# Kernel optimization log

Hardware: AMD Instinct MI355X
Metric: run time of the kernel (lower is better)

The kernel has to match this reference:

```python
import jax, jax.numpy as jnp
import numpy as np

D_MODEL = 2048
N_HEADS = 16
D_HEAD = 128
B = 2
S = 2048


def setup_inputs() -> dict:
    key = jax.random.key(0)
    ks = jax.random.split(key, 9)
    sc_in = 1.0 / np.sqrt(D_MODEL)
    sc_hd = 1.0 / np.sqrt(N_HEADS * D_HEAD)
    return {
        "x": jax.random.normal(ks[0], (B, S, D_MODEL), dtype=jnp.float32),
        "Wq": jax.random.normal(ks[1], (D_MODEL, N_HEADS * D_HEAD), dtype=jnp.float32) * sc_in,
        "bq": jax.random.normal(ks[2], (N_HEADS * D_HEAD,), dtype=jnp.float32) * 0.01,
        "Wk": jax.random.normal(ks[3], (D_MODEL, N_HEADS * D_HEAD), dtype=jnp.float32) * sc_in,
        "bk": jax.random.normal(ks[4], (N_HEADS * D_HEAD,), dtype=jnp.float32) * 0.01,
        "Wv": jax.random.normal(ks[5], (D_MODEL, N_HEADS * D_HEAD), dtype=jnp.float32) * sc_in,
        "bv": jax.random.normal(ks[6], (N_HEADS * D_HEAD,), dtype=jnp.float32) * 0.01,
        "Wo": jax.random.normal(ks[7], (N_HEADS * D_HEAD, D_MODEL), dtype=jnp.float32) * sc_hd,
        "bo": jax.random.normal(ks[8], (D_MODEL,), dtype=jnp.float32) * 0.01,
    }


def reference(x, Wq, bq, Wk, bk, Wv, bv, Wo, bo):
    b, s, _ = x.shape
    # projections -> [b, s, h, d] -> [b, h, s, d]
    q = (x @ Wq + bq).reshape(b, s, N_HEADS, D_HEAD).transpose(0, 2, 1, 3)
    k = (x @ Wk + bk).reshape(b, s, N_HEADS, D_HEAD).transpose(0, 2, 1, 3)
    v = (x @ Wv + bv).reshape(b, s, N_HEADS, D_HEAD).transpose(0, 2, 1, 3)
    scale = 1.0 / jnp.sqrt(jnp.asarray(D_HEAD, dtype=x.dtype))
    scores = jnp.einsum("bhsd,bhtd->bhst", q, k) * scale  # [b,h,s,s]
    causal = jnp.triu(jnp.ones((s, s), dtype=bool), k=1)
    scores = jnp.where(causal, jnp.asarray(-jnp.inf, dtype=scores.dtype), scores)
    attn = jax.nn.softmax(scores, axis=-1)
    ctx = jnp.einsum("bhst,bhtd->bhsd", attn, v)  # [b,h,s,d]
    ctx = ctx.transpose(0, 2, 1, 3).reshape(b, s, N_HEADS * D_HEAD)
    return ctx @ Wo + bo
```

## Files before the change

### kernel.cpp

```cpp
#include <hip/hip_runtime.h>
#include <hip/hip_bf16.h>
#include <stdint.h>

#define S_LEN  2048
#define DMODEL 2048
#define NHEADS 16
#define DHEAD  128
#define NBATCH 2
#define MROWS  (NBATCH * S_LEN)

typedef __bf16 bf16_t;
typedef __bf16 bf16x8 __attribute__((ext_vector_type(8)));
typedef float  f32x4  __attribute__((ext_vector_type(4)));
typedef float  f32x16 __attribute__((ext_vector_type(16)));

#define MFMA_BF16(A, B, C) __builtin_amdgcn_mfma_f32_16x16x32_bf16((A), (B), (C), 0, 0, 0)
#define MFMA32(A, B, C)    __builtin_amdgcn_mfma_f32_32x32x16_bf16((A), (B), (C), 0, 0, 0)

__device__ __forceinline__ void gload_lds16(const void* g, void* l) {
  __builtin_amdgcn_global_load_lds(
      (__attribute__((address_space(1))) uint32_t*)(uintptr_t)g,
      (__attribute__((address_space(3))) uint32_t*)l,
      16, 0, 0);
}

__device__ __forceinline__ unsigned pk2(float lo, float hi) {
  const unsigned short a = __builtin_bit_cast(unsigned short, (bf16_t)lo);
  const unsigned short b = __builtin_bit_cast(unsigned short, (bf16_t)hi);
  return (unsigned)a | ((unsigned)b << 16);
}

__global__ __launch_bounds__(256) void cast_kernel(const float* __restrict__ X,
                                                   bf16_t* __restrict__ Xb) {
  const int i = blockIdx.x * 256 + threadIdx.x;
  const f32x4 a = ((const f32x4*)X)[2 * i];
  const f32x4 b = ((const f32x4*)X)[2 * i + 1];
  bf16x8 o;
#pragma unroll
  for (int j = 0; j < 4; ++j) { o[j] = (bf16_t)a[j]; o[j + 4] = (bf16_t)b[j]; }
  ((bf16x8*)Xb)[i] = o;
}

__global__ __launch_bounds__(256) void transpose_cast(
    const float* __restrict__ W0, const float* __restrict__ W1,
    const float* __restrict__ W2, const float* __restrict__ W3,
    bf16_t* __restrict__ T0, bf16_t* __restrict__ T1,
    bf16_t* __restrict__ T2, bf16_t* __restrict__ T3) {
  const float* W; bf16_t* T;
  switch (blockIdx.z) {
    case 0:  W = W0; T = T0; break;
    case 1:  W = W1; T = T1; break;
    case 2:  W = W2; T = T2; break;
    default: W = W3; T = T3; break;
  }
  __shared__ float tile[64][65];
  const int r0 = blockIdx.y * 64;
  const int c0 = blockIdx.x * 64;
  const int tx = threadIdx.x & 63;
  const int ty = threadIdx.x >> 6;
#pragma unroll
  for (int i = 0; i < 16; ++i) {
    const int r = ty + i * 4;
    tile[r][tx] = W[(size_t)(r0 + r) * DMODEL + c0 + tx];
  }
  __syncthreads();
#pragma unroll
  for (int i = 0; i < 16; ++i) {
    const int r = ty + i * 4;
    T[(size_t)(c0 + r) * DMODEL + r0 + tx] = (bf16_t)tile[tx][r];
  }
}

__global__ __launch_bounds__(256) void transpose_v(const bf16_t* __restrict__ V,
                                                   bf16_t* __restrict__ VT) {
  __shared__ bf16_t tile[64 * 64];
  const int bh = blockIdx.z;
  const int s0 = blockIdx.x * 64;
  const int d0 = blockIdx.y * 64;
  const bf16_t* src = V + ((size_t)bh * S_LEN + s0) * DHEAD + d0;
#pragma unroll
  for (int i = 0; i < 2; ++i) {
    const int v = threadIdx.x + i * 256;
    const int r = v >> 3, ch = v & 7;
    *(bf16x8*)&tile[r * 64 + ((ch ^ ((r >> 3) & 7)) << 3)] =
        *(const bf16x8*)(src + (size_t)r * DHEAD + ch * 8);
  }
  __syncthreads();
  bf16_t* dst = VT + ((size_t)bh * DHEAD + d0) * S_LEN + s0;
#pragma unroll
  for (int i = 0; i < 2; ++i) {
    const int v = threadIdx.x + i * 256;
    const int d = v >> 3, j = v & 7;
    bf16x8 o;
#pragma unroll
    for (int e = 0; e < 8; ++e) {
      const int row = j * 8 + e;
      o[e] = tile[row * 64 + (((d >> 3) ^ j) << 3) + (d & 7)];
    }
    *(bf16x8*)(dst + (size_t)d * S_LEN + j * 8) = o;
  }
}

#define VMCNT(N) asm volatile("s_waitcnt vmcnt(" #N ")" ::: "memory")

#define QPHASE(T, P, N) do {                                                     \
  VMCNT(N);                                                                      \
  __builtin_amdgcn_s_barrier();                                                  \
  asm volatile("" ::: "memory");                                                 \
  {                                                                              \
    const char* regA = lds + ((T) & 1) * 65536 + ((P) >> 1) * 32768;             \
    const char* regB = regA + 16384;                                             \
    if (((P) & 1) == 0) {                                                        \
      _Pragma("unroll")                                                          \
      for (int j = 0; j < 4; ++j)                                                \
        bf[j] = *(const bf16x8*)(regB + (wn * 64 + j * 16 + l16) * 64 + g * 16); \
    }                                                                            \
    bf16x8 af[4];                                                                \
    _Pragma("unroll")                                                            \
    for (int i = 0; i < 4; ++i)                                                  \
      af[i] = *(const bf16x8*)(regA + (wm * 128 + (((P) & 1) * 4 + i) * 16 + l16) * 64 + g * 16); \
    stage((T) + 1, (P));                                                         \
    __builtin_amdgcn_s_setprio(1);                                               \
    _Pragma("unroll")                                                            \
    for (int i = 0; i < 4; ++i) {                                                \
      _Pragma("unroll")                                                          \
      for (int j = 0; j < 4; ++j)                                                \
        acc[((P) & 1) * 4 + i][j] =                                              \
            MFMA_BF16(af[i], bf[j], acc[((P) & 1) * 4 + i][j]);                  \
    }                                                                            \
    __builtin_amdgcn_s_setprio(0);                                               \
  }                                                                              \
} while (0)

__global__ __launch_bounds__(512, 2) void gemm_qkv(
    const bf16_t* __restrict__ Xb,
    const bf16_t* __restrict__ WqT, const bf16_t* __restrict__ WkT,
    const bf16_t* __restrict__ WvT,
    const float* __restrict__ bq, const float* __restrict__ bk,
    const float* __restrict__ bv,
    bf16_t* __restrict__ Qg, bf16_t* __restrict__ Kg, bf16_t* __restrict__ Vg) {
  __shared__ __align__(16) char lds[2 * 65536];

  const int tid  = threadIdx.x;
  const int lane = tid & 63;
  const int w    = tid >> 6;
  const int g    = lane >> 4;
  const int l16  = lane & 15;
  const int wm   = w >> 2;
  const int wn   = w & 3;

  const int bid = blockIdx.x;
  const int wg  = (bid & 7) * 48 + (bid >> 3);
  const int mi  = wg / 24;
  const int ni  = wg % 24;
  const int z0  = ni >> 3;
  const bf16_t* Bt = (z0 == 0) ? WqT : (z0 == 1) ? WkT : WvT;
  const bf16_t* Abase = Xb + (size_t)mi * 256 * DMODEL;
  const bf16_t* Bbase = Bt + (size_t)(ni & 7) * 256 * DMODEL;

  f32x4 acc[8][4];
#pragma unroll
  for (int i = 0; i < 8; ++i)
#pragma unroll
    for (int j = 0; j < 4; ++j) acc[i][j] = (f32x4){0.f, 0.f, 0.f, 0.f};

  auto stage = [&](int tile, int p) {
    if (tile >= DMODEL / 64) return;
    const int kh = p >> 1, mat = p & 1;
    const int kt = tile * 64 + kh * 32;
    const bf16_t* src = mat ? Bbase : Abase;
    char* dstbase = lds + (tile & 1) * 65536 + kh * 32768 + mat * 16384;
#pragma unroll
    for (int jj = 0; jj < 2; ++jj) {
      const int c = jj * 512 + tid;
      gload_lds16(src + (size_t)(c >> 2) * DMODEL + kt + (c & 3) * 8,
                  dstbase + (jj * 512 + (tid & ~63)) * 16);
    }
  };

  stage(0, 0); stage(0, 1); stage(0, 2); stage(0, 3);

  bf16x8 bf[4];
  for (int t = 0; t < DMODEL / 64 - 1; ++t) {
    QPHASE(t, 0, 4);
    QPHASE(t, 1, 6);
    QPHASE(t, 2, 4);
    QPHASE(t, 3, 6);
  }
  {
    const int t = DMODEL / 64 - 1;
    QPHASE(t, 0, 4);
    QPHASE(t, 1, 4);
    QPHASE(t, 2, 2);
    QPHASE(t, 3, 0);
  }

  const float* bias = (z0 == 0) ? bq : (z0 == 1) ? bk : bv;
  bf16_t* outb      = (z0 == 0) ? Qg : (z0 == 1) ? Kg : Vg;
#pragma unroll
  for (int i = 0; i < 8; ++i) {
#pragma unroll
    for (int j = 0; j < 4; ++j) {
      const int nloc = (ni & 7) * 256 + wn * 64 + j * 16 + l16;
      const float bb = bias[nloc];
      const int h = nloc >> 7, d = nloc & (DHEAD - 1);
#pragma unroll
      for (int r = 0; r < 4; ++r) {
        const int mrow = mi * 256 + wm * 128 + i * 16 + g * 4 + r;
        const int b = mrow >> 11, s = mrow & (S_LEN - 1);
        outb[((size_t)(b * NHEADS + h) * S_LEN + s) * DHEAD + d] =
            (bf16_t)(acc[i][j][r] + bb);
      }
    }
  }
}

template <int MODE>
__device__ __forceinline__ void gemm8_body(const bf16_t* __restrict__ A,
                                           const bf16_t* __restrict__ Bt,
                                           const float* __restrict__ bias,
                                           void* __restrict__ out) {
  __shared__ __align__(16) char lds8[2 * 49152];
  const int tid  = threadIdx.x;
  const int lane = tid & 63;
  const int w    = tid >> 6;
  const int g    = lane >> 4;
  const int l16  = lane & 15;
  const int wm   = w >> 2;
  const int wn   = w & 3;
  const int m0   = blockIdx.y * 128;
  const int n0   = blockIdx.x * 256;

  f32x4 acc[4][4];
#pragma unroll
  for (int i = 0; i < 4; ++i)
#pragma unroll
    for (int j = 0; j < 4; ++j) acc[i][j] = (f32x4){0.f, 0.f, 0.f, 0.f};

  const int st_r0 = tid >> 3;
  const int st_ch = tid & 7;

  auto stage = [&](int tile, int r) {
    if (tile >= DMODEL / 64) return;
    const int kt = tile << 6;
    char* db = lds8 + (tile & 1) * 49152 + r * 16384 + w * 1024;
    const bf16_t* sb = (r == 0) ? (A + (size_t)m0 * DMODEL + kt)
                                : (Bt + (size_t)(n0 + ((r - 1) << 7)) * DMODEL + kt);
#pragma unroll
    for (int jj = 0; jj < 2; ++jj) {
      const int row = jj * 64 + st_r0;
      gload_lds16(sb + (size_t)row * DMODEL + ((st_ch ^ (row & 7)) << 3),
                  db + jj * 8192);
    }
  };

  stage(0, 0); stage(0, 1); stage(0, 2); stage(1, 0);
  asm volatile("s_waitcnt vmcnt(2)" ::: "memory");
  __builtin_amdgcn_s_barrier();

#pragma unroll 2
  for (int t = 0; t < DMODEL / 64; ++t) {
    const char* cb = lds8 + (t & 1) * 49152;
    bf16x8 af[4][2], b0[2][2], b1[2][2];
#pragma unroll
    for (int i = 0; i < 4; ++i) {
      const int row = wm * 64 + i * 16 + l16;
      const char* rp = cb + row * 128;
#pragma unroll
      for (int ks = 0; ks < 2; ++ks)
        af[i][ks] = *(const bf16x8*)(rp + ((((ks << 2) | g) ^ (row & 7)) << 4));
    }
#pragma unroll
    for (int j = 0; j < 2; ++j) {
      const int row = (wn & 1) * 64 + j * 16 + l16;
      const char* rp = cb + 16384 + (wn >> 1) * 16384 + row * 128;
#pragma unroll
      for (int ks = 0; ks < 2; ++ks)
        b0[j][ks] = *(const bf16x8*)(rp + ((((ks << 2) | g) ^ (row & 7)) << 4));
    }
    stage(t + 1, 1); stage(t + 1, 2);
    __builtin_amdgcn_s_barrier();
    asm volatile("s_waitcnt lgkmcnt(0)" ::: "memory");
    __builtin_amdgcn_s_setprio(1);
#pragma unroll
    for (int i = 0; i < 4; ++i)
#pragma unroll
      for (int j = 0; j < 2; ++j) {
        acc[i][j] = MFMA_BF16(af[i][0], b0[j][0], acc[i][j]);
        acc[i][j] = MFMA_BF16(af[i][1], b0[j][1], acc[i][j]);
      }
    __builtin_amdgcn_s_setprio(0);
    __builtin_amdgcn_s_barrier();
#pragma unroll
    for (int j = 0; j < 2; ++j) {
      const int row = (wn & 1) * 64 + (j + 2) * 16 + l16;
      const char* rp = cb + 16384 + (wn >> 1) * 16384 + row * 128;
#pragma unroll
      for (int ks = 0; ks < 2; ++ks)
        b1[j][ks] = *(const bf16x8*)(rp + ((((ks << 2) | g) ^ (row & 7)) << 4));
    }
    stage(t + 2, 0);
    __builtin_amdgcn_s_barrier();
    asm volatile("s_waitcnt lgkmcnt(0)" ::: "memory");
    __builtin_amdgcn_s_setprio(1);
#pragma unroll
    for (int i = 0; i < 4; ++i)
#pragma unroll
      for (int j = 0; j < 2; ++j) {
        acc[i][j + 2] = MFMA_BF16(af[i][0], b1[j][0], acc[i][j + 2]);
        acc[i][j + 2] = MFMA_BF16(af[i][1], b1[j][1], acc[i][j + 2]);
      }
    __builtin_amdgcn_s_setprio(0);
    if (t < DMODEL / 64 - 2) asm volatile("s_waitcnt vmcnt(2)" ::: "memory");
    else                     asm volatile("s_waitcnt vmcnt(0)" ::: "memory");
    __builtin_amdgcn_s_barrier();
  }

#pragma unroll
  for (int i = 0; i < 4; ++i) {
#pragma unroll
    for (int j = 0; j < 4; ++j) {
      const int n    = n0 + wn * 64 + j * 16 + l16;
      const float bb = bias[n];
#pragma unroll
      for (int r = 0; r < 4; ++r) {
        const int m   = m0 + wm * 64 + i * 16 + g * 4 + r;
        const float v = acc[i][j][r] + bb;
        if (MODE == 0) {
          const int b = m >> 11, s = m & (S_LEN - 1);
          const int h = n >> 7,  d = n & (DHEAD - 1);
          ((bf16_t*)out)[((size_t)(b * NHEADS + h) * S_LEN + s) * DHEAD + d] = (bf16_t)v;
        } else {
          ((float*)out)[(size_t)m * DMODEL + n] = v;
        }
      }
    }
  }
}

__global__ __launch_bounds__(512, 2) void gemm_out(
    const bf16_t* __restrict__ Ctx, const bf16_t* __restrict__ WoT,
    const float* __restrict__ bo, float* __restrict__ out) {
  gemm8_body<1>(Ctx, WoT, bo, out);
}

#define KLDS_BYTES (64 * 272)
#define VLDS_BYTES (128 * 144)
#define BUF_BYTES  (KLDS_BYTES + VLDS_BYTES)

__global__ __launch_bounds__(256, 2) void attn_kernel(
    const bf16_t* __restrict__ Qg, const bf16_t* __restrict__ Kg,
    const bf16_t* __restrict__ VTg, bf16_t* __restrict__ ctx) {
  __shared__ __align__(16) char ldsbuf[2][BUF_BYTES];
  __shared__ float lbuf[4][32];

  const int tid  = threadIdx.x;
  const int lane = tid & 63;
  const int w    = tid >> 6;
  const int l31  = lane & 31;
  const int hi   = lane >> 5;

  const int id   = blockIdx.x;
  const int bh   = id & 31;
  const int jraw = id >> 5;
  const int j    = (jraw < 8) ? jraw : 23 - jraw;
  const int q0   = j * 128;
  const int qw   = q0 + w * 32;
  const int tq   = (qw + 31) >> 6;
  const int NT   = (q0 + 128) >> 6;

  const size_t bho = (size_t)bh * S_LEN * DHEAD;
  const bf16_t* Qb  = Qg + bho;
  const bf16_t* Kb  = Kg + bho;
  const bf16_t* VTb = VTg + bho;

  bf16x8 qreg[8];
#pragma unroll
  for (int s = 0; s < 8; ++s)
    qreg[s] = *(const bf16x8*)(Qb + (size_t)(qw + l31) * DHEAD + s * 16 + hi * 8);

  f32x16 oacc[4];
#pragma unroll
  for (int d0 = 0; d0 < 4; ++d0)
#pragma unroll
    for (int e = 0; e < 16; ++e) oacc[d0][e] = 0.f;

  float m = -1e30f, lsum = 0.f;
  const float sc2 = 0.12751751135f;

  bf16x8 kst[4], vst[4];
#pragma unroll
  for (int i = 0; i < 4; ++i) {
    const int c = tid + i * 256;
    kst[i] = *(const bf16x8*)(Kb + (size_t)(c >> 4) * DHEAD + (c & 15) * 8);
    vst[i] = *(const bf16x8*)(VTb + (size_t)(c >> 3) * S_LEN + (c & 7) * 8);
  }
#pragma unroll
  for (int i = 0; i < 4; ++i) {
    const int c  = tid + i * 256;
    const int kr = c >> 4, kc = c & 15;
    *(bf16x8*)(ldsbuf[0] + kr * 272 + ((kc ^ ((kr >> 3) & 3)) << 4)) = kst[i];
    const int vr = c >> 3, vc = c & 7;
    *(bf16x8*)(ldsbuf[0] + KLDS_BYTES + vr * 144 + ((vc ^ ((vr >> 3) & 3)) << 4)) = vst[i];
  }
  __syncthreads();

  for (int t = 0; t < NT; ++t) {
    const int kt = t << 6;
    const char* bK = ldsbuf[t & 1];
    const char* bV = bK + KLDS_BYTES;
    const bool hn = (t + 1 < NT);
    if (hn) {
#pragma unroll
      for (int i = 0; i < 4; ++i) {
        const int c = tid + i * 256;
        kst[i] = *(const bf16x8*)(Kb + (size_t)(kt + 64 + (c >> 4)) * DHEAD + (c & 15) * 8);
        vst[i] = *(const bf16x8*)(VTb + (size_t)(c >> 3) * S_LEN + kt + 64 + (c & 7) * 8);
      }
    }

    if (t <= tq) {
      f32x16 stt[2];
#pragma unroll
      for (int kh = 0; kh < 2; ++kh)
#pragma unroll
        for (int e = 0; e < 16; ++e) stt[kh][e] = 0.f;
#pragma unroll
      for (int kh = 0; kh < 2; ++kh) {
        const int row = kh * 32 + l31;
        const char* rb = bK + row * 272;
        const int swz = ((row >> 3) & 3) << 4;
#pragma unroll
        for (int s = 0; s < 8; ++s) {
          const bf16x8 kf = *(const bf16x8*)(rb + ((((s << 1) | hi) << 4) ^ swz));
          stt[kh] = MFMA32(kf, qreg[s], stt[kh]);
        }
      }
      if (t == tq) {
        const int qg = qw + l31;
#pragma unroll
        for (int kh = 0; kh < 2; ++kh)
#pragma unroll
          for (int r = 0; r < 16; ++r) {
            const int kv = kt + kh * 32 + (r & 3) + 8 * (r >> 2) + 4 * hi;
            stt[kh][r] = (kv > qg) ? -1e30f : stt[kh][r];
          }
      }
      float pm = stt[0][0];
#pragma unroll
      for (int kh = 0; kh < 2; ++kh)
#pragma unroll
        for (int r = 0; r < 16; ++r)
          if (kh | r) pm = fmaxf(pm, stt[kh][r]);
      pm = fmaxf(pm, __shfl_xor(pm, 32));
      const float pmax = pm * sc2;
      if (!__all(pmax <= m + 8.f)) {
        const float mn   = fmaxf(m, pmax);
        const float corr = __builtin_amdgcn_exp2f(m - mn);
        m = mn;
        lsum *= corr;
        if (!hi) lbuf[w][l31] = corr;
#pragma unroll
        for (int r = 0; r < 16; ++r) {
          const float cr = lbuf[w][(r & 3) + 8 * (r >> 2) + 4 * hi];
#pragma unroll
          for (int d0 = 0; d0 < 4; ++d0) oacc[d0][r] *= cr;
        }
      }
      float rs = 0.f;
#pragma unroll
      for (int kh = 0; kh < 2; ++kh)
#pragma unroll
        for (int r = 0; r < 16; ++r) {
          const float p = __builtin_amdgcn_exp2f(__builtin_fmaf(stt[kh][r], sc2, -m));
          stt[kh][r] = p;
          rs += p;
        }
      rs += __shfl_xor(rs, 32);
      lsum += rs;
      unsigned pw_[2][8];
#pragma unroll
      for (int kh = 0; kh < 2; ++kh)
#pragma unroll
        for (int jj = 0; jj < 8; ++jj)
          pw_[kh][jj] = pk2(stt[kh][2 * jj], stt[kh][2 * jj + 1]);
      bf16x8 pa[4];
#pragma unroll
      for (int kh = 0; kh < 2; ++kh)
#pragma unroll
        for (int c2 = 0; c2 < 2; ++c2) {
          const unsigned o0 = pw_[kh][4 * c2 + 0], o1 = pw_[kh][4 * c2 + 1];
          const unsigned o2 = pw_[kh][4 * c2 + 2], o3 = pw_[kh][4 * c2 + 3];
          const unsigned p0 = (unsigned)__shfl_xor((int)o0, 32);
          const unsigned p1 = (unsigned)__shfl_xor((int)o1, 32);
          const unsigned p2 = (unsigned)__shfl_xor((int)o2, 32);
          const unsigned p3 = (unsigned)__shfl_xor((int)o3, 32);
          union { unsigned u[4]; bf16x8 v; } uu;
          uu.u[0] = hi ? p2 : o0;
          uu.u[1] = hi ? p3 : o1;
          uu.u[2] = hi ? o2 : p0;
          uu.u[3] = hi ? o3 : p1;
          pa[2 * kh + c2] = uu.v;
        }
#pragma unroll
      for (int d0 = 0; d0 < 4; ++d0) {
        const int row = d0 * 32 + l31;
        const char* rb = bV + row * 144;
        const int swz = ((row >> 3) & 3) << 4;
#pragma unroll
        for (int ks = 0; ks < 4; ++ks) {
          const bf16x8 vb = *(const bf16x8*)(rb + ((((ks << 1) | hi) << 4) ^ swz));
          oacc[d0] = MFMA32(pa[ks], vb, oacc[d0]);
        }
      }
    }
    __syncthreads();
    if (hn) {
      char* nB = ldsbuf[(t + 1) & 1];
#pragma unroll
      for (int i = 0; i < 4; ++i) {
        const int c  = tid + i * 256;
        const int kr = c >> 4, kc = c & 15;
        *(bf16x8*)(nB + kr * 272 + ((kc ^ ((kr >> 3) & 3)) << 4)) = kst[i];
        const int vr = c >> 3, vc = c & 7;
        *(bf16x8*)(nB + KLDS_BYTES + vr * 144 + ((vc ^ ((vr >> 3) & 3)) << 4)) = vst[i];
      }
    }
    __syncthreads();
  }

  if (!hi) lbuf[w][l31] = 1.0f / lsum;
  const int b = bh >> 4, h = bh & 15;
#pragma unroll
  for (int r = 0; r < 16; ++r) {
    const int cro = (r & 3) + 8 * (r >> 2) + 4 * hi;
    const float li = lbuf[w][cro];
    const size_t base = ((size_t)(b * S_LEN + qw + cro)) * DMODEL + h * DHEAD;
#pragma unroll
    for (int d0 = 0; d0 < 4; ++d0)
      ctx[base + d0 * 32 + l31] = (bf16_t)(oacc[d0][r] * li);
  }
}

extern "C" void kernel_launch(void* const* d_in, const int* in_sizes, int n_in,
                              void* d_out, int out_size, void* d_ws, size_t ws_size,
                              hipStream_t stream) {
  const float* x  = (const float*)d_in[0];
  const float* Wq = (const float*)d_in[1];
  const float* bq = (const float*)d_in[2];
  const float* Wk = (const float*)d_in[3];
  const float* bk = (const float*)d_in[4];
  const float* Wv = (const float*)d_in[5];
  const float* bv = (const float*)d_in[6];
  const float* Wo = (const float*)d_in[7];
  const float* bo = (const float*)d_in[8];

  char* ws = (char*)d_ws;
  const size_t MB = 1ull << 20;
  bf16_t* Xb  = (bf16_t*)(ws + 0);
  bf16_t* VTg = (bf16_t*)(ws + 0);
  bf16_t* WqT = (bf16_t*)(ws + 16 * MB);
  bf16_t* WkT = (bf16_t*)(ws + 24 * MB);
  bf16_t* WvT = (bf16_t*)(ws + 32 * MB);
  bf16_t* WoT = (bf16_t*)(ws + 40 * MB);
  bf16_t* Qg  = (bf16_t*)(ws + 48 * MB);
  bf16_t* Kg  = (bf16_t*)(ws + 64 * MB);
  bf16_t* Vg  = (bf16_t*)(ws + 80 * MB);
  bf16_t* Ctx = (bf16_t*)(ws + 96 * MB);
  if (ws_size < 112 * MB) return;

  cast_kernel<<<dim3(MROWS * DMODEL / (256 * 8)), 256, 0, stream>>>(x, Xb);
  transpose_cast<<<dim3(32, 32, 4), 256, 0, stream>>>(Wq, Wk, Wv, Wo, WqT, WkT, WvT, WoT);
  gemm_qkv<<<dim3(384), 512, 0, stream>>>(
      Xb, WqT, WkT, WvT, bq, bk, bv, Qg, Kg, Vg);
  transpose_v<<<dim3(32, 2, 32), 256, 0, stream>>>(Vg, VTg);
  attn_kernel<<<dim3(512), 256, 0, stream>>>(Qg, Kg, VTg, Ctx);
  gemm_out<<<dim3(DMODEL / 256, MROWS / 128), 512, 0, stream>>>(Ctx, WoT, bo, (float*)d_out);
}
```

Measured before the change: 246.4 us.

## Restructure QKV GEMM main loop into quadrant schedule with swizzled LDS tiles

Replaces the four-phase K-split pipeline of the QKV projection GEMM with a schedule that keeps each 64-wide k tile whole in LDS. The warp tile is split into four quadrants of MFMAs, and global-to-LDS loads are interleaved between them: B for the next tile, and A two tiles ahead. The LDS layout changes to 128-byte rows with an XOR chunk swizzle, meant to cut bank conflicts on the ds_read fragments. The intent is better overlap of memory traffic with MFMA work, at the cost of more barriers per tile and more fragment registers.

After: 245.6 us. About the same (-0.3%).

```diff
diff --git a/kernel.cpp b/kernel.cpp
--- a/kernel.cpp
+++ b/kernel.cpp
@@ -101,37 +101,6 @@
   }
 }
 
-#define VMCNT(N) asm volatile("s_waitcnt vmcnt(" #N ")" ::: "memory")
-
-#define QPHASE(T, P, N) do {                                                     \
-  VMCNT(N);                                                                      \
-  __builtin_amdgcn_s_barrier();                                                  \
-  asm volatile("" ::: "memory");                                                 \
-  {                                                                              \
-    const char* regA = lds + ((T) & 1) * 65536 + ((P) >> 1) * 32768;             \
-    const char* regB = regA + 16384;                                             \
-    if (((P) & 1) == 0) {                                                        \
-      _Pragma("unroll")                                                          \
-      for (int j = 0; j < 4; ++j)                                                \
-        bf[j] = *(const bf16x8*)(regB + (wn * 64 + j * 16 + l16) * 64 + g * 16); \
-    }                                                                            \
-    bf16x8 af[4];                                                                \
-    _Pragma("unroll")                                                            \
-    for (int i = 0; i < 4; ++i)                                                  \
-      af[i] = *(const bf16x8*)(regA + (wm * 128 + (((P) & 1) * 4 + i) * 16 + l16) * 64 + g * 16); \
-    stage((T) + 1, (P));                                                         \
-    __builtin_amdgcn_s_setprio(1);                                               \
-    _Pragma("unroll")                                                            \
-    for (int i = 0; i < 4; ++i) {                                                \
-      _Pragma("unroll")                                                          \
-      for (int j = 0; j < 4; ++j)                                                \
-        acc[((P) & 1) * 4 + i][j] =                                              \
-            MFMA_BF16(af[i], bf[j], acc[((P) & 1) * 4 + i][j]);                  \
-    }                                                                            \
-    __builtin_amdgcn_s_setprio(0);                                               \
-  }                                                                              \
-} while (0)
-
 __global__ __launch_bounds__(512, 2) void gemm_qkv(
     const bf16_t* __restrict__ Xb,
     const bf16_t* __restrict__ WqT, const bf16_t* __restrict__ WkT,
@@ -148,6 +117,7 @@
   const int l16  = lane & 15;
   const int wm   = w >> 2;
   const int wn   = w & 3;
+  const int NTILES = DMODEL / 64;
 
   const int bid = blockIdx.x;
   const int wg  = (bid & 7) * 48 + (bid >> 3);
@@ -164,35 +134,112 @@
 #pragma unroll
     for (int j = 0; j < 4; ++j) acc[i][j] = (f32x4){0.f, 0.f, 0.f, 0.f};
 
-  auto stage = [&](int tile, int p) {
-    if (tile >= DMODEL / 64) return;
-    const int kh = p >> 1, mat = p & 1;
-    const int kt = tile * 64 + kh * 32;
-    const bf16_t* src = mat ? Bbase : Abase;
-    char* dstbase = lds + (tile & 1) * 65536 + kh * 32768 + mat * 16384;
+  auto stage = [&](int tile, int mat, int half) {
+    if (tile >= NTILES) return;
+    const bf16_t* gb = (mat ? Bbase : Abase) + (size_t)(half * 128) * DMODEL + tile * 64;
+    char* unit = lds + (tile & 1) * 65536 + mat * 32768 + half * 16384;
 #pragma unroll
     for (int jj = 0; jj < 2; ++jj) {
-      const int c = jj * 512 + tid;
-      gload_lds16(src + (size_t)(c >> 2) * DMODEL + kt + (c & 3) * 8,
-                  dstbase + (jj * 512 + (tid & ~63)) * 16);
+      const int c   = jj * 512 + tid;
+      const int row = c >> 3;
+      const int ch  = c & 7;
+      gload_lds16(gb + (size_t)row * DMODEL + ((ch ^ (row & 7)) << 3),
+                  unit + (jj * 512 + (tid & ~63)) * 16);
     }
   };
 
-  stage(0, 0); stage(0, 1); stage(0, 2); stage(0, 3);
-
-  bf16x8 bf[4];
-  for (int t = 0; t < DMODEL / 64 - 1; ++t) {
-    QPHASE(t, 0, 4);
-    QPHASE(t, 1, 6);
-    QPHASE(t, 2, 4);
-    QPHASE(t, 3, 6);
-  }
-  {
-    const int t = DMODEL / 64 - 1;
-    QPHASE(t, 0, 4);
-    QPHASE(t, 1, 4);
-    QPHASE(t, 2, 2);
-    QPHASE(t, 3, 0);
+  stage(0, 0, 0); stage(0, 0, 1); stage(0, 1, 0); stage(0, 1, 1);
+  stage(1, 0, 0); stage(1, 0, 1);
+  asm volatile("s_waitcnt vmcnt(4)" ::: "memory");
+  __builtin_amdgcn_s_barrier();
+
+  for (int t = 0; t < NTILES; ++t) {
+    const char* cbA = lds + (t & 1) * 65536;
+    const char* cbB = cbA + 32768;
+    bf16x8 af[4][2], bf0[2][2], bf1[2][2];
+
+#pragma unroll
+    for (int i = 0; i < 4; ++i) {
+      const int row = wm * 128 + i * 16 + l16;
+#pragma unroll
+      for (int ks = 0; ks < 2; ++ks)
+        af[i][ks] = *(const bf16x8*)(cbA + row * 128 + ((((ks << 2) | g) ^ (row & 7)) << 4));
+    }
+#pragma unroll
+    for (int j = 0; j < 2; ++j) {
+      const int row = wn * 64 + j * 16 + l16;
+#pragma unroll
+      for (int ks = 0; ks < 2; ++ks)
+        bf0[j][ks] = *(const bf16x8*)(cbB + row * 128 + ((((ks << 2) | g) ^ (row & 7)) << 4));
+    }
+    stage(t + 1, 1, 0);
+    __builtin_amdgcn_s_barrier();
+    asm volatile("s_waitcnt lgkmcnt(0)" ::: "memory");
+    __builtin_amdgcn_s_setprio(1);
+#pragma unroll
+    for (int i = 0; i < 4; ++i)
+#pragma unroll
+      for (int j = 0; j < 2; ++j) {
+        acc[i][j] = MFMA_BF16(af[i][0], bf0[j][0], acc[i][j]);
+        acc[i][j] = MFMA_BF16(af[i][1], bf0[j][1], acc[i][j]);
+      }
+    __builtin_amdgcn_s_setprio(0);
+    __builtin_amdgcn_s_barrier();
+
+#pragma unroll
+    for (int j = 0; j < 2; ++j) {
+      const int row = wn * 64 + (j + 2) * 16 + l16;
+#pragma unroll
+      for (int ks = 0; ks < 2; ++ks)
+        bf1[j][ks] = *(const bf16x8*)(cbB + row * 128 + ((((ks << 2) | g) ^ (row & 7)) << 4));
+    }
+    stage(t + 1, 1, 1);
+    __builtin_amdgcn_s_barrier();
+    asm volatile("s_waitcnt lgkmcnt(0)" ::: "memory");
+    __builtin_amdgcn_s_setprio(1);
+#pragma unroll
+    for (int i = 0; i < 4; ++i)
+#pragma unroll
+      for (int j = 0; j < 2; ++j) {
+        acc[i][j + 2] = MFMA_BF16(af[i][0], bf1[j][0], acc[i][j + 2]);
+        acc[i][j + 2] = MFMA_BF16(af[i][1], bf1[j][1], acc[i][j + 2]);
+      }
+    __builtin_amdgcn_s_setprio(0);
+    __builtin_amdgcn_s_barrier();
+
+#pragma unroll
+    for (int i = 0; i < 4; ++i) {
+      const int row = wm * 128 + (i + 4) * 16 + l16;
+#pragma unroll
+      for (int ks = 0; ks < 2; ++ks)
+        af[i][ks] = *(const bf16x8*)(cbA + row * 128 + ((((ks << 2) | g) ^ (row & 7)) << 4));
+    }
+    __builtin_amdgcn_s_barrier();
+    asm volatile("s_waitcnt lgkmcnt(0)" ::: "memory");
+    __builtin_amdgcn_s_setprio(1);
+#pragma unroll
+    for (int i = 0; i < 4; ++i)
+#pragma unroll
+      for (int j = 0; j < 2; ++j) {
+        acc[i + 4][j + 2] = MFMA_BF16(af[i][0], bf1[j][0], acc[i + 4][j + 2]);
+        acc[i + 4][j + 2] = MFMA_BF16(af[i][1], bf1[j][1], acc[i + 4][j + 2]);
+      }
+    __builtin_amdgcn_s_setprio(0);
+    __builtin_amdgcn_s_barrier();
+
+    stage(t + 2, 0, 0); stage(t + 2, 0, 1);
+    __builtin_amdgcn_s_setprio(1);
+#pragma unroll
+    for (int i = 0; i < 4; ++i)
+#pragma unroll
+      for (int j = 0; j < 2; ++j) {
+        acc[i + 4][j] = MFMA_BF16(af[i][0], bf0[j][0], acc[i + 4][j]);
+        acc[i + 4][j] = MFMA_BF16(af[i][1], bf0[j][1], acc[i + 4][j]);
+      }
+    __builtin_amdgcn_s_setprio(0);
+    if (t < NTILES - 2) { asm volatile("s_waitcnt vmcnt(4)" ::: "memory"); }
+    else                { asm volatile("s_waitcnt vmcnt(0)" ::: "memory"); }
+    __builtin_amdgcn_s_barrier();
   }
 
   const float* bias = (z0 == 0) ? bq : (z0 == 1) ? bk : bv;
```
